# Kernel optimization log

Hardware: AMD Instinct MI355X
Metric: run time of the kernel (lower is better)

The kernel has to match this reference:

```python
import jax, jax.numpy as jnp
import numpy as np

C = 1024       # num_channels
HD = 64        # head_dim
NH = C // HD   # 16 heads
LMAX = 1024    # max segment length (static)
EPS = 1.1920929e-07  # torch.finfo(float32).eps, nn.RMSNorm default


def setup_inputs() -> dict:
    key = jax.random.key(0)
    ks = jax.random.split(key, 6)
    # 16 ragged segments, lengths alternate 768/256, sum = 8192
    lengths = np.tile(np.array([768, 256], dtype=np.int32), 8)
    cu = np.concatenate([[0], np.cumsum(lengths)]).astype(np.int32)
    T = int(cu[-1])
    s = 1.0 / np.sqrt(C)
    return {
        "x": jax.random.normal(ks[0], (T, C), jnp.float32),
        "cu_seqlens": jnp.asarray(cu),
        "Wq": jax.random.normal(ks[1], (C, C), jnp.float32) * s,
        "bq": jnp.zeros((C,), jnp.float32),
        "Wk": jax.random.normal(ks[2], (C, C), jnp.float32) * s,
        "bk": jnp.zeros((C,), jnp.float32),
        "Wv": jax.random.normal(ks[3], (C, C), jnp.float32) * s,
        "bv": jnp.zeros((C,), jnp.float32),
        "qn_w": jnp.ones((HD,), jnp.float32),
        "kn_w": jnp.ones((HD,), jnp.float32),
        "Wo": jax.random.normal(ks[4], (C, C), jnp.float32) * s,
        "bo": jnp.zeros((C,), jnp.float32),
    }


def _rmsnorm(h, w):
    # RMSNorm over last (head_dim) axis with learned scale
    return h * jax.lax.rsqrt(jnp.mean(h * h, axis=-1, keepdims=True) + EPS) * w


def reference(x, cu_seqlens, Wq, bq, Wk, bk, Wv, bv, qn_w, kn_w, Wo, bo):
    T = x.shape[0]
    q = (x @ Wq.T + bq).reshape(T, NH, HD)
    k = (x @ Wk.T + bk).reshape(T, NH, HD)
    v = (x @ Wv.T + bv).reshape(T, NH, HD)
    q = _rmsnorm(q, qn_w)
    k = _rmsnorm(k, kn_w)

    # gather ragged segments into padded [B, LMAX, H, D]
    starts = cu_seqlens[:-1]
    lens = cu_seqlens[1:] - starts
    pos = jnp.arange(LMAX, dtype=cu_seqlens.dtype)
    idx = starts[:, None] + pos[None, :]      # [B, LMAX]
    valid = pos[None, :] < lens[:, None]      # [B, LMAX]
    gidx = jnp.where(valid, idx, 0)
    qp, kp, vp = q[gidx], k[gidx], v[gidx]    # [B, LMAX, H, D]

    scale = 1.0 / np.sqrt(HD)
    scores = jnp.einsum('blhd,bshd->bhls', qp, kp) * scale
    scores = jnp.where(valid[:, None, None, :], scores, -1e9)  # mask pad keys
    probs = jax.nn.softmax(scores, axis=-1)
    op = jnp.einsum('bhls,bshd->blhd', probs, vp)  # [B, LMAX, H, D]

    # scatter valid tokens back to packed layout; pad rows dropped (idx=T OOB)
    sidx = jnp.where(valid, idx, T).reshape(-1)
    out = jnp.zeros((T, NH, HD), x.dtype).at[sidx].set(
        op.reshape(-1, NH, HD), mode='drop')
    return out.reshape(T, C) @ Wo.T + bo
```

## Files before the change

### kernel.cpp

```cpp
#include <hip/hip_runtime.h>

typedef unsigned short u16;
typedef unsigned int   u32;

typedef __bf16 bf16x8_t __attribute__((ext_vector_type(8)));
typedef bf16x8_t bf16x8 __attribute__((may_alias));
typedef float f32x4_t __attribute__((ext_vector_type(4)));
typedef f32x4_t f32x4 __attribute__((may_alias));
typedef u32 u32x4_t __attribute__((ext_vector_type(4)));
typedef u32x4_t u32x4 __attribute__((may_alias));
typedef u32 u32x2_t __attribute__((ext_vector_type(2)));
typedef u32x2_t u32x2 __attribute__((may_alias));

__device__ __forceinline__ u16 f2b(float f) {
  __bf16 h = (__bf16)f; u16 u; __builtin_memcpy(&u, &h, 2); return u;
}
__device__ __forceinline__ float b2f(u16 u) {
  u32 i = ((u32)u) << 16; float f; __builtin_memcpy(&f, &i, 4); return f;
}
__device__ __forceinline__ bf16x8_t cvt8(const float* p) {
  f32x4_t a = *(const f32x4*)p;
  f32x4_t b = *(const f32x4*)(p + 4);
  bf16x8_t v;
  v[0]=(__bf16)a[0]; v[1]=(__bf16)a[1]; v[2]=(__bf16)a[2]; v[3]=(__bf16)a[3];
  v[4]=(__bf16)b[0]; v[5]=(__bf16)b[1]; v[6]=(__bf16)b[2]; v[7]=(__bf16)b[3];
  return v;
}
typedef __attribute__((address_space(1))) const void* as1cv;
typedef __attribute__((address_space(3))) void* as3v;
__device__ __forceinline__ void gld16(const u16* g, u16* l) {
  __builtin_amdgcn_global_load_lds((as1cv)g, (as3v)l, 16, 0, 0);
}

#define EPS 1.1920929e-07f

#define WSZ (1024 * 1024)
__global__ __launch_bounds__(256) void cvt_pack(
    const float* __restrict__ x, const float* __restrict__ wq,
    const float* __restrict__ wk, const float* __restrict__ wv,
    const float* __restrict__ wo, u16* __restrict__ dst, int nx)
{
  int idx4 = blockIdx.x * 256 + threadIdx.x;
  const int total4 = (nx + 4 * WSZ) >> 2;
  for (; idx4 < total4; idx4 += gridDim.x * 256) {
    int i = idx4 << 2;
    const float* src;
    if (i < nx) src = x + i;
    else {
      int o = i - nx;
      if      (o <     WSZ) src = wq + o;
      else if (o < 2 * WSZ) src = wk + o - WSZ;
      else if (o < 3 * WSZ) src = wv + o - 2 * WSZ;
      else                  src = wo + o - 3 * WSZ;
    }
    f32x4_t v = *(const f32x4*)src;
    u32x2_t p;
    p[0] = (u32)f2b(v[0]) | ((u32)f2b(v[1]) << 16);
    p[1] = (u32)f2b(v[2]) | ((u32)f2b(v[3]) << 16);
    *(u32x2*)(dst + i) = p;
  }
}

#define BK 32
template<int NORM, int CF32>
__global__ __launch_bounds__(256, 2) void gemm_bt2(
    const u16* __restrict__ A, const u16* __restrict__ Bm,
    const float* __restrict__ bias0, const float* __restrict__ bias1, const float* __restrict__ bias2,
    const float* __restrict__ qn, const float* __restrict__ kn,
    void* __restrict__ C, int M, int K, int ldc)
{
  __shared__ alignas(16) u16 As[128 * BK];
  __shared__ alignas(16) u16 Bs[128 * BK];
  const int t = threadIdx.x;
  const int lane = t & 63, wave = t >> 6;
  const int quad = lane >> 4, col = lane & 15;
  const int m0 = blockIdx.x * 128, n0 = blockIdx.y * 128;
  const int seg = n0 >> 10, nl0 = n0 & 1023;
  const float* bias = seg == 0 ? bias0 : (seg == 1 ? bias1 : bias2);
  const int wm = (wave >> 1) * 64, wn = (wave & 1) * 64;

  const int lrow = t >> 2;
  const int lcol = (t & 3) * 8;
  const u16* ga0 = A  + (size_t)(m0 + lrow) * K + lcol;
  const u16* ga1 = A  + (size_t)(m0 + 64 + lrow) * K + lcol;
  const u16* gb0 = Bm + (size_t)(n0 + lrow) * K + lcol;
  const u16* gb1 = Bm + (size_t)(n0 + 64 + lrow) * K + lcol;
  u16* lA0 = As + t * 8;
  u16* lA1 = As + 64 * BK + t * 8;
  u16* lB0 = Bs + t * 8;
  u16* lB1 = Bs + 64 * BK + t * 8;

  f32x4_t acc[4][4] = {};
  for (int k0 = 0; k0 < K; k0 += BK) {
    __syncthreads();
    gld16(ga0 + k0, lA0);
    gld16(ga1 + k0, lA1);
    gld16(gb0 + k0, lB0);
    gld16(gb1 + k0, lB1);
    __syncthreads();
    bf16x8 af[4], bfr[4];
#pragma unroll
    for (int i = 0; i < 4; ++i) {
      af[i]  = *(const bf16x8*)(As + (wm + i * 16 + col) * BK + quad * 8);
      bfr[i] = *(const bf16x8*)(Bs + (wn + i * 16 + col) * BK + quad * 8);
    }
#pragma unroll
    for (int i = 0; i < 4; ++i)
#pragma unroll
      for (int j = 0; j < 4; ++j)
        acc[i][j] = __builtin_amdgcn_mfma_f32_16x16x32_bf16(af[i], bfr[j], acc[i][j], 0, 0, 0);
  }

  float bz[4], wz[4];
#pragma unroll
  for (int j = 0; j < 4; ++j) {
    bz[j] = bias[nl0 + wn + j * 16 + col];
    if (NORM) wz[j] = (seg == 0 ? qn : kn)[j * 16 + col];
  }
  const bool donorm = NORM && seg < 2;
#pragma unroll
  for (int i = 0; i < 4; ++i) {
#pragma unroll
    for (int rr = 0; rr < 4; ++rr) {
      int gm = m0 + wm + i * 16 + quad * 4 + rr;
      float v[4];
#pragma unroll
      for (int j = 0; j < 4; ++j) v[j] = acc[i][j][rr] + bz[j];
      if (donorm) {
        float ss = v[0]*v[0] + v[1]*v[1] + v[2]*v[2] + v[3]*v[3];
        ss += __shfl_xor(ss, 1);
        ss += __shfl_xor(ss, 2);
        ss += __shfl_xor(ss, 4);
        ss += __shfl_xor(ss, 8);
        float sc = rsqrtf(ss * (1.0f / 64.0f) + EPS);
#pragma unroll
        for (int j = 0; j < 4; ++j) v[j] *= sc * wz[j];
      }
      if (gm < M) {
#pragma unroll
        for (int j = 0; j < 4; ++j) {
          int gn = n0 + wn + j * 16 + col;
          if (CF32) ((float*)C)[(size_t)gm * ldc + gn] = v[j];
          else      ((u16*)C)[(size_t)gm * ldc + gn] = f2b(v[j]);
        }
      }
    }
  }
}

template<int AF32, int CF32>
__global__ __launch_bounds__(256, 2) void gemm_bt(
    const void* __restrict__ Av,
    const float* __restrict__ B0, const float* __restrict__ B1, const float* __restrict__ B2,
    const float* __restrict__ bias0, const float* __restrict__ bias1, const float* __restrict__ bias2,
    void* __restrict__ C, int M, int K, int ldc)
{
  __shared__ alignas(16) u16 As[128 * BK];
  __shared__ alignas(16) u16 Bs[128 * BK];
  const int t = threadIdx.x;
  const int lane = t & 63, wave = t >> 6;
  const int quad = lane >> 4, col = lane & 15;
  const int m0 = blockIdx.x * 128, n0 = blockIdx.y * 128;
  const int seg = n0 >> 10;
  const float* B    = seg == 0 ? B0    : (seg == 1 ? B1    : B2);
  const float* bias = seg == 0 ? bias0 : (seg == 1 ? bias1 : bias2);
  const int nl0 = n0 & 1023;
  const int wm = (wave >> 1) * 64, wn = (wave & 1) * 64;
  const int lrow = t >> 2;
  const int lcol = (t & 3) * 8;
  int ar0 = m0 + lrow;      if (ar0 >= M) ar0 = M - 1;
  int ar1 = m0 + 64 + lrow; if (ar1 >= M) ar1 = M - 1;
  const float* bp0 = B + (size_t)(nl0 + lrow) * K + lcol;
  const float* bp1 = B + (size_t)(nl0 + 64 + lrow) * K + lcol;
  const float* apf0 = (const float*)Av + (size_t)ar0 * K + lcol;
  const float* apf1 = (const float*)Av + (size_t)ar1 * K + lcol;
  const u16*   aph0 = (const u16*)Av   + (size_t)ar0 * K + lcol;
  const u16*   aph1 = (const u16*)Av   + (size_t)ar1 * K + lcol;
  u16* lA0 = As + t * 8;
  u16* lA1 = As + 64 * BK + t * 8;
  u16* lB0 = Bs + t * 8;
  u16* lB1 = Bs + 64 * BK + t * 8;

  f32x4_t acc[4][4] = {};
  for (int k0 = 0; k0 < K; k0 += BK) {
    bf16x8_t va0, va1, vb0, vb1;
    if (AF32) { va0 = cvt8(apf0 + k0); va1 = cvt8(apf1 + k0); }
    else {
      u32x4_t r0 = *(const u32x4*)(aph0 + k0);
      u32x4_t r1 = *(const u32x4*)(aph1 + k0);
      __builtin_memcpy(&va0, &r0, 16);
      __builtin_memcpy(&va1, &r1, 16);
    }
    vb0 = cvt8(bp0 + k0);
    vb1 = cvt8(bp1 + k0);
    __syncthreads();
    *(bf16x8*)lA0 = va0; *(bf16x8*)lA1 = va1;
    *(bf16x8*)lB0 = vb0; *(bf16x8*)lB1 = vb1;
    __syncthreads();
    bf16x8 af[4], bfr[4];
#pragma unroll
    for (int i = 0; i < 4; ++i) {
      af[i]  = *(const bf16x8*)(As + (wm + i * 16 + col) * BK + quad * 8);
      bfr[i] = *(const bf16x8*)(Bs + (wn + i * 16 + col) * BK + quad * 8);
    }
#pragma unroll
    for (int i = 0; i < 4; ++i)
#pragma unroll
      for (int j = 0; j < 4; ++j)
        acc[i][j] = __builtin_amdgcn_mfma_f32_16x16x32_bf16(af[i], bfr[j], acc[i][j], 0, 0, 0);
  }
#pragma unroll
  for (int j = 0; j < 4; ++j) {
    int gn = n0 + wn + j * 16 + col;
    float bz = bias[nl0 + wn + j * 16 + col];
#pragma unroll
    for (int i = 0; i < 4; ++i) {
#pragma unroll
      for (int rr = 0; rr < 4; ++rr) {
        int gm = m0 + wm + i * 16 + quad * 4 + rr;
        if (gm < M) {
          float v = acc[i][j][rr] + bz;
          if (CF32) ((float*)C)[(size_t)gm * ldc + gn] = v;
          else      ((u16*)C)[(size_t)gm * ldc + gn] = f2b(v);
        }
      }
    }
  }
}

__global__ __launch_bounds__(256) void rmsnorm_qk(
    u16* __restrict__ qkv, const float* __restrict__ qn, const float* __restrict__ kn, int T)
{
  int gid = blockIdx.x * 256 + threadIdx.x;
  int row = gid >> 4, sub = gid & 15;
  if (row >= 2 * T * 16) return;
  int which = row >= T * 16;
  int r = which ? row - T * 16 : row;
  int tok = r >> 4, head = r & 15;
  u16* p = qkv + (size_t)tok * 3072 + which * 1024 + head * 64 + sub * 4;
  u16 d0 = p[0], d1 = p[1], d2 = p[2], d3 = p[3];
  float f0 = b2f(d0), f1 = b2f(d1), f2v = b2f(d2), f3 = b2f(d3);
  float ss = f0 * f0 + f1 * f1 + f2v * f2v + f3 * f3;
  ss += __shfl_xor(ss, 1);
  ss += __shfl_xor(ss, 2);
  ss += __shfl_xor(ss, 4);
  ss += __shfl_xor(ss, 8);
  float sc = rsqrtf(ss * (1.0f / 64.0f) + EPS);
  const float* w = which ? kn : qn;
  p[0] = f2b(f0 * sc * w[sub * 4 + 0]);
  p[1] = f2b(f1 * sc * w[sub * 4 + 1]);
  p[2] = f2b(f2v * sc * w[sub * 4 + 2]);
  p[3] = f2b(f3 * sc * w[sub * 4 + 3]);
}

#define SKS 68
#define SVS 68
#define SPS 68
__global__ __launch_bounds__(256, 4) void attn_fwd(
    const u16* __restrict__ qkv, const int* __restrict__ cu, u16* __restrict__ out)
{
  __shared__ alignas(16) u16 Ks[64 * SKS];
  __shared__ alignas(16) u16 Vts[64 * SVS];
  __shared__ alignas(16) u16 Ps[8 * 16 * SPS];
  const int seq = blockIdx.z, head = blockIdx.x, qt = blockIdx.y;
  const int start = cu[seq], len = cu[seq + 1] - start;
  const int q0 = qt * 128;
  if (q0 >= len) return;
  const int t = threadIdx.x;
  const int lane = t & 63, wave = t >> 6, quad = lane >> 4, col = lane & 15;

  const int rA = q0 + wave * 16 + col, rB = rA + 64;
  const u16* qpA = qkv + (size_t)(start + (rA < len ? rA : len - 1)) * 3072 + head * 64 + quad * 8;
  const u16* qpB = qkv + (size_t)(start + (rB < len ? rB : len - 1)) * 3072 + head * 64 + quad * 8;
  bf16x8 qfA0 = *(const bf16x8*)qpA;
  bf16x8 qfA1 = *(const bf16x8*)(qpA + 32);
  bf16x8 qfB0 = *(const bf16x8*)qpB;
  bf16x8 qfB1 = *(const bf16x8*)(qpB + 32);

  f32x4_t accOA[4] = {}, accOB[4] = {};
  float lA[4] = {}, lB[4] = {};
  const float SC = 0.125f * 1.44269504089f;

  const int sp = t >> 3, dc = t & 7;
  const int kc = sp & 15, kh = sp >> 4;
  const int keyA = kc + 32 * kh;
  u16* ksA = Ks + keyA * SKS + dc * 8;
  u16* ksB = Ks + (keyA + 16) * SKS + dc * 8;
  const int vcol = kc * 4 + 2 * kh;
  const size_t kvbase = 1024 + head * 64 + dc * 8;

  const int nkv = (len + 63) >> 6;
  u32x4_t rkA, rkB, rvA, rvB;
  {
    int ta = start + (keyA      < len ? keyA      : len - 1);
    int tb = start + (keyA + 16 < len ? keyA + 16 : len - 1);
    const u16* pa = qkv + (size_t)ta * 3072 + kvbase;
    const u16* pb2 = qkv + (size_t)tb * 3072 + kvbase;
    rkA = *(const u32x4*)pa;   rvA = *(const u32x4*)(pa + 1024);
    rkB = *(const u32x4*)pb2;  rvB = *(const u32x4*)(pb2 + 1024);
  }

  for (int it = 0; it < nkv; ++it) {
    const int k0 = it << 6;
    __syncthreads();
    *(u32x4*)ksA = rkA;
    *(u32x4*)ksB = rkB;
    {
      const u16* a = (const u16*)&rvA;
      const u16* b = (const u16*)&rvB;
#pragma unroll
      for (int j = 0; j < 8; ++j) {
        u32 pk = (u32)a[j] | ((u32)b[j] << 16);
        *(u32*)(Vts + (dc * 8 + j) * SVS + vcol) = pk;
      }
    }
    __syncthreads();
    if (it + 1 < nkv) {
      int kb0 = k0 + 64;
      int ta = start + (kb0 + keyA      < len ? kb0 + keyA      : len - 1);
      int tb = start + (kb0 + keyA + 16 < len ? kb0 + keyA + 16 : len - 1);
      const u16* pa = qkv + (size_t)ta * 3072 + kvbase;
      const u16* pb2 = qkv + (size_t)tb * 3072 + kvbase;
      rkA = *(const u32x4*)pa;   rvA = *(const u32x4*)(pa + 1024);
      rkB = *(const u32x4*)pb2;  rvB = *(const u32x4*)(pb2 + 1024);
    }

    f32x4_t sgA[4], sgB[4];
#pragma unroll
    for (int g = 0; g < 4; ++g) {
      bf16x8 kb0 = *(const bf16x8*)(Ks + (g*16 + col) * SKS + quad * 8);
      bf16x8 kb1 = *(const bf16x8*)(Ks + (g*16 + col) * SKS + 32 + quad * 8);
      f32x4_t sA = {}, sB = {};
      sA = __builtin_amdgcn_mfma_f32_16x16x32_bf16(qfA0, kb0, sA, 0, 0, 0);
      sB = __builtin_amdgcn_mfma_f32_16x16x32_bf16(qfB0, kb0, sB, 0, 0, 0);
      sA = __builtin_amdgcn_mfma_f32_16x16x32_bf16(qfA1, kb1, sA, 0, 0, 0);
      sB = __builtin_amdgcn_mfma_f32_16x16x32_bf16(qfB1, kb1, sB, 0, 0, 0);
      sgA[g] = sA; sgB[g] = sB;
    }

    const bool full = (k0 + 64 <= len);
    bool vg[4];
#pragma unroll
    for (int g = 0; g < 4; ++g) vg[g] = full || (k0 + g*16 + col) < len;
    u16* pwA = Ps + wave * (16 * SPS);
    u16* pwB = Ps + (4 + wave) * (16 * SPS);
#pragma unroll
    for (int r = 0; r < 4; ++r) {
      u16 peA[4], peB[4];
#pragma unroll
      for (int g = 0; g < 4; ++g) {
        float pA = exp2f(sgA[g][r] * SC);
        float pB = exp2f(sgB[g][r] * SC);
        peA[g] = vg[g] ? f2b(pA) : (u16)0;
        peB[g] = vg[g] ? f2b(pB) : (u16)0;
      }
      lA[r] += (b2f(peA[0]) + b2f(peA[1])) + (b2f(peA[2]) + b2f(peA[3]));
      lB[r] += (b2f(peB[0]) + b2f(peB[1])) + (b2f(peB[2]) + b2f(peB[3]));
      u32x2_t wA, wB;
      wA[0] = (u32)peA[0] | ((u32)peA[1] << 16);
      wA[1] = (u32)peA[2] | ((u32)peA[3] << 16);
      wB[0] = (u32)peB[0] | ((u32)peB[1] << 16);
      wB[1] = (u32)peB[2] | ((u32)peB[3] << 16);
      *(u32x2*)(pwA + (quad*4 + r) * SPS + col * 4) = wA;
      *(u32x2*)(pwB + (quad*4 + r) * SPS + col * 4) = wB;
    }
    __threadfence_block();

    bf16x8 pfA0 = *(const bf16x8*)(pwA + col * SPS + quad * 8);
    bf16x8 pfA1 = *(const bf16x8*)(pwA + col * SPS + 32 + quad * 8);
    bf16x8 pfB0 = *(const bf16x8*)(pwB + col * SPS + quad * 8);
    bf16x8 pfB1 = *(const bf16x8*)(pwB + col * SPS + 32 + quad * 8);
#pragma unroll
    for (int c = 0; c < 4; ++c) {
      bf16x8 vf0 = *(const bf16x8*)(Vts + (c*16 + col) * SVS + quad * 8);
      bf16x8 vf1 = *(const bf16x8*)(Vts + (c*16 + col) * SVS + 32 + quad * 8);
      accOA[c] = __builtin_amdgcn_mfma_f32_16x16x32_bf16(pfA0, vf0, accOA[c], 0, 0, 0);
      accOB[c] = __builtin_amdgcn_mfma_f32_16x16x32_bf16(pfB0, vf0, accOB[c], 0, 0, 0);
      accOA[c] = __builtin_amdgcn_mfma_f32_16x16x32_bf16(pfA1, vf1, accOA[c], 0, 0, 0);
      accOB[c] = __builtin_amdgcn_mfma_f32_16x16x32_bf16(pfB1, vf1, accOB[c], 0, 0, 0);
    }
  }

#pragma unroll
  for (int r = 0; r < 4; ++r) {
    float sA = lA[r], sB = lB[r];
    sA += __shfl_xor(sA, 1); sB += __shfl_xor(sB, 1);
    sA += __shfl_xor(sA, 2); sB += __shfl_xor(sB, 2);
    sA += __shfl_xor(sA, 4); sB += __shfl_xor(sB, 4);
    sA += __shfl_xor(sA, 8); sB += __shfl_xor(sB, 8);
    int rowA = q0 + wave * 16 + quad * 4 + r;
    int rowB = rowA + 64;
    if (rowA < len) {
      float inv = 1.0f / sA;
      u16* op = out + (size_t)(start + rowA) * 1024 + head * 64 + col;
      op[0]  = f2b(accOA[0][r] * inv);
      op[16] = f2b(accOA[1][r] * inv);
      op[32] = f2b(accOA[2][r] * inv);
      op[48] = f2b(accOA[3][r] * inv);
    }
    if (rowB < len) {
      float inv = 1.0f / sB;
      u16* op = out + (size_t)(start + rowB) * 1024 + head * 64 + col;
      op[0]  = f2b(accOB[0][r] * inv);
      op[16] = f2b(accOB[1][r] * inv);
      op[32] = f2b(accOB[2][r] * inv);
      op[48] = f2b(accOB[3][r] * inv);
    }
  }
}

__global__ void ws_too_small_sentinel(float* out) {
  if (threadIdx.x == 0 && blockIdx.x == 0) out[0] = 1024.0f;
}

extern "C" void kernel_launch(void* const* d_in, const int* in_sizes, int n_in,
                              void* d_out, int out_size, void* d_ws, size_t ws_size,
                              hipStream_t stream) {
  const float* x  = (const float*)d_in[0];
  const int*   cu = (const int*)d_in[1];
  const float* Wq = (const float*)d_in[2];
  const float* bq = (const float*)d_in[3];
  const float* Wk = (const float*)d_in[4];
  const float* bk = (const float*)d_in[5];
  const float* Wv = (const float*)d_in[6];
  const float* bv = (const float*)d_in[7];
  const float* qn = (const float*)d_in[8];
  const float* kn = (const float*)d_in[9];
  const float* Wo = (const float*)d_in[10];
  const float* bo = (const float*)d_in[11];

  const int T = in_sizes[0] / 1024;
  const int nseq = in_sizes[1] - 1;

  const size_t need_fast = ((size_t)T * 5120 + 4 * WSZ) * 2;
  const size_t need_fall = (size_t)T * 4096 * 2;

  u16* qkv  = (u16*)d_ws;
  u16* attn = qkv + (size_t)T * 3072;
  dim3 blk(256);

  if (ws_size >= need_fast) {
    u16* xb   = attn + (size_t)T * 1024;
    u16* wqkv = xb + (size_t)T * 1024;
    u16* wo   = wqkv + 3 * WSZ;
    cvt_pack<<<dim3(1024), blk, 0, stream>>>(x, Wq, Wk, Wv, Wo, xb, T * 1024);
    gemm_bt2<1, 0><<<dim3((T + 127) / 128, 24), blk, 0, stream>>>(
        xb, wqkv, bq, bk, bv, qn, kn, qkv, T, 1024, 3072);
    attn_fwd<<<dim3(16, 8, nseq), blk, 0, stream>>>(qkv, cu, attn);
    gemm_bt2<0, 1><<<dim3((T + 127) / 128, 8), blk, 0, stream>>>(
        attn, wo, bo, bo, bo, qn, kn, d_out, T, 1024, 1024);
  } else if (ws_size >= need_fall) {
    gemm_bt<1, 0><<<dim3((T + 127) / 128, 24), blk, 0, stream>>>(
        x, Wq, Wk, Wv, bq, bk, bv, qkv, T, 1024, 3072);
    rmsnorm_qk<<<dim3((2 * T * 256 + 255) / 256), blk, 0, stream>>>(qkv, qn, kn, T);
    attn_fwd<<<dim3(16, 8, nseq), blk, 0, stream>>>(qkv, cu, attn);
    gemm_bt<0, 1><<<dim3((T + 127) / 128, 8), blk, 0, stream>>>(
        attn, Wo, Wo, Wo, bo, bo, bo, d_out, T, 1024, 1024);
  } else {
    ws_too_small_sentinel<<<1, 64, 0, stream>>>((float*)d_out);
  }
}
```

Measured before the change: 266.9 us.

## Replace bf16 GEMM with 256x256-tile, 8-wave, double-buffered swizzled-LDS kernel

Replaces the 128x128 tile, BK=32 GEMM with a 512-thread kernel that computes 256x256 output tiles using BK=64 K-steps. The next K-tile's global-to-LDS loads are double-buffered and interleaved with the MFMA phases. LDS columns are XOR-swizzled to avoid bank conflicts, and workgroup IDs are remapped for L2 locality. This targets the low arithmetic intensity and the exposed load latency of the old GEMM, at the cost of 128KB of LDS per block, heavy register use, and far fewer blocks: 32x12 for QKV and 32x4 for the output projection.

Result: slower. 288.3 us (+8.0%).

```diff
diff --git a/kernel.cpp b/kernel.cpp
--- a/kernel.cpp
+++ b/kernel.cpp
@@ -61,71 +61,118 @@
   }
 }
 
-#define BK 32
 template<int NORM, int CF32>
-__global__ __launch_bounds__(256, 2) void gemm_bt2(
+__global__ __launch_bounds__(512, 2) void gemm8(
     const u16* __restrict__ A, const u16* __restrict__ Bm,
     const float* __restrict__ bias0, const float* __restrict__ bias1, const float* __restrict__ bias2,
     const float* __restrict__ qn, const float* __restrict__ kn,
     void* __restrict__ C, int M, int K, int ldc)
 {
-  __shared__ alignas(16) u16 As[128 * BK];
-  __shared__ alignas(16) u16 Bs[128 * BK];
+  __shared__ alignas(16) u16 lds[65536];
   const int t = threadIdx.x;
   const int lane = t & 63, wave = t >> 6;
   const int quad = lane >> 4, col = lane & 15;
-  const int m0 = blockIdx.x * 128, n0 = blockIdx.y * 128;
-  const int seg = n0 >> 10, nl0 = n0 & 1023;
+  const int wm = wave >> 2, wn = wave & 3;
+
+  const int nwg = gridDim.x * gridDim.y;
+  int fid = blockIdx.y * gridDim.x + blockIdx.x;
+  int wg = (nwg & 7) ? fid : ((fid & 7) * (nwg >> 3) + (fid >> 3));
+  const int m0 = (wg % gridDim.x) * 256;
+  const int n0 = (wg / gridDim.x) * 256;
+
+  const int srow = t >> 3;
+  const int sx = ((t & 7) ^ (srow & 7)) << 3;
+  const u16* asrc[2][2];
+  const u16* bsrc[2][2];
+#pragma unroll
+  for (int h = 0; h < 2; ++h)
+#pragma unroll
+    for (int q = 0; q < 2; ++q) {
+      int ar = m0 + h * 128 + q * 64 + srow; if (ar >= M) ar = M - 1;
+      asrc[h][q] = A  + (size_t)ar * K + sx;
+      int br = n0 + h * 128 + q * 64 + srow;
+      bsrc[h][q] = Bm + (size_t)br * K + sx;
+    }
+  const int dst8 = t * 8;
+
+#pragma unroll
+  for (int h = 0; h < 2; ++h)
+#pragma unroll
+    for (int q = 0; q < 2; ++q) {
+      gld16(asrc[h][q],         lds +         h * 8192 + q * 4096 + dst8);
+      gld16(bsrc[h][q], lds + 32768 + h * 8192 + q * 4096 + dst8);
+    }
+  __syncthreads();
+
+  f32x4_t acc[8][4] = {};
+  const int nt = K >> 6;
+  for (int k = 0; k < nt; ++k) {
+    const int d = k & 1, nk = k + 1, nd = nk & 1;
+    const int koff = nk << 6;
+    const u16* Ab = lds +         (2 * d + wm) * 8192;
+    const u16* Bb = lds + 32768 + (2 * d + (wn >> 1)) * 8192;
+    const int browb = ((wn & 1) * 64) << 6;
+    bf16x8 bfr[4];
+#pragma unroll
+    for (int p = 0; p < 4; ++p) {
+      const int g = p & 1, ks = p >> 1;
+      const int ck = (((ks * 4 + quad) ^ (col & 7)) << 3);
+      if (g == 0) {
+#pragma unroll
+        for (int nj = 0; nj < 4; ++nj)
+          bfr[nj] = *(const bf16x8*)(Bb + browb + ((nj * 16 + col) << 6) + ck);
+      }
+      bf16x8 af[4];
+#pragma unroll
+      for (int i = 0; i < 4; ++i)
+        af[i] = *(const bf16x8*)(Ab + (((g * 4 + i) * 16 + col) << 6) + ck);
+      if (nk < nt) {
+        if (p == 0) {
+          gld16(asrc[0][0] + koff, lds + (2 * nd) * 8192 + dst8);
+          gld16(asrc[0][1] + koff, lds + (2 * nd) * 8192 + 4096 + dst8);
+        } else if (p == 1) {
+          gld16(asrc[1][0] + koff, lds + (2 * nd + 1) * 8192 + dst8);
+          gld16(asrc[1][1] + koff, lds + (2 * nd + 1) * 8192 + 4096 + dst8);
+        } else if (p == 2) {
+          gld16(bsrc[0][0] + koff, lds + 32768 + (2 * nd) * 8192 + dst8);
+          gld16(bsrc[0][1] + koff, lds + 32768 + (2 * nd) * 8192 + 4096 + dst8);
+        } else {
+          gld16(bsrc[1][0] + koff, lds + 32768 + (2 * nd + 1) * 8192 + dst8);
+          gld16(bsrc[1][1] + koff, lds + 32768 + (2 * nd + 1) * 8192 + 4096 + dst8);
+        }
+      }
+      __builtin_amdgcn_s_barrier();
+      __builtin_amdgcn_s_setprio(1);
+#pragma unroll
+      for (int i = 0; i < 4; ++i)
+#pragma unroll
+        for (int nj = 0; nj < 4; ++nj)
+          acc[g * 4 + i][nj] = __builtin_amdgcn_mfma_f32_16x16x32_bf16(
+              af[i], bfr[nj], acc[g * 4 + i][nj], 0, 0, 0);
+      __builtin_amdgcn_s_setprio(0);
+      if (p < 3) __builtin_amdgcn_s_barrier();
+    }
+    __syncthreads();
+  }
+
+  const int gnb = n0 + wn * 64;
+  const int seg = gnb >> 10, nl = gnb & 1023;
   const float* bias = seg == 0 ? bias0 : (seg == 1 ? bias1 : bias2);
-  const int wm = (wave >> 1) * 64, wn = (wave & 1) * 64;
-
-  const int lrow = t >> 2;
-  const int lcol = (t & 3) * 8;
-  const u16* ga0 = A  + (size_t)(m0 + lrow) * K + lcol;
-  const u16* ga1 = A  + (size_t)(m0 + 64 + lrow) * K + lcol;
-  const u16* gb0 = Bm + (size_t)(n0 + lrow) * K + lcol;
-  const u16* gb1 = Bm + (size_t)(n0 + 64 + lrow) * K + lcol;
-  u16* lA0 = As + t * 8;
-  u16* lA1 = As + 64 * BK + t * 8;
-  u16* lB0 = Bs + t * 8;
-  u16* lB1 = Bs + 64 * BK + t * 8;
-
-  f32x4_t acc[4][4] = {};
-  for (int k0 = 0; k0 < K; k0 += BK) {
-    __syncthreads();
-    gld16(ga0 + k0, lA0);
-    gld16(ga1 + k0, lA1);
-    gld16(gb0 + k0, lB0);
-    gld16(gb1 + k0, lB1);
-    __syncthreads();
-    bf16x8 af[4], bfr[4];
-#pragma unroll
-    for (int i = 0; i < 4; ++i) {
-      af[i]  = *(const bf16x8*)(As + (wm + i * 16 + col) * BK + quad * 8);
-      bfr[i] = *(const bf16x8*)(Bs + (wn + i * 16 + col) * BK + quad * 8);
-    }
-#pragma unroll
-    for (int i = 0; i < 4; ++i)
-#pragma unroll
-      for (int j = 0; j < 4; ++j)
-        acc[i][j] = __builtin_amdgcn_mfma_f32_16x16x32_bf16(af[i], bfr[j], acc[i][j], 0, 0, 0);
-  }
-
   float bz[4], wz[4];
 #pragma unroll
-  for (int j = 0; j < 4; ++j) {
-    bz[j] = bias[nl0 + wn + j * 16 + col];
-    if (NORM) wz[j] = (seg == 0 ? qn : kn)[j * 16 + col];
+  for (int nj = 0; nj < 4; ++nj) {
+    bz[nj] = bias[nl + nj * 16 + col];
+    if (NORM) wz[nj] = (seg == 0 ? qn : kn)[nj * 16 + col];
   }
   const bool donorm = NORM && seg < 2;
 #pragma unroll
-  for (int i = 0; i < 4; ++i) {
+  for (int mi = 0; mi < 8; ++mi) {
 #pragma unroll
     for (int rr = 0; rr < 4; ++rr) {
-      int gm = m0 + wm + i * 16 + quad * 4 + rr;
+      int gm = m0 + wm * 128 + mi * 16 + quad * 4 + rr;
       float v[4];
 #pragma unroll
-      for (int j = 0; j < 4; ++j) v[j] = acc[i][j][rr] + bz[j];
+      for (int nj = 0; nj < 4; ++nj) v[nj] = acc[mi][nj][rr] + bz[nj];
       if (donorm) {
         float ss = v[0]*v[0] + v[1]*v[1] + v[2]*v[2] + v[3]*v[3];
         ss += __shfl_xor(ss, 1);
@@ -134,20 +181,21 @@
         ss += __shfl_xor(ss, 8);
         float sc = rsqrtf(ss * (1.0f / 64.0f) + EPS);
 #pragma unroll
-        for (int j = 0; j < 4; ++j) v[j] *= sc * wz[j];
+        for (int nj = 0; nj < 4; ++nj) v[nj] *= sc * wz[nj];
       }
       if (gm < M) {
 #pragma unroll
-        for (int j = 0; j < 4; ++j) {
-          int gn = n0 + wn + j * 16 + col;
-          if (CF32) ((float*)C)[(size_t)gm * ldc + gn] = v[j];
-          else      ((u16*)C)[(size_t)gm * ldc + gn] = f2b(v[j]);
+        for (int nj = 0; nj < 4; ++nj) {
+          int gn = gnb + nj * 16 + col;
+          if (CF32) ((float*)C)[(size_t)gm * ldc + gn] = v[nj];
+          else      ((u16*)C)[(size_t)gm * ldc + gn] = f2b(v[nj]);
         }
       }
     }
   }
 }
 
+#define BK 32
 template<int AF32, int CF32>
 __global__ __launch_bounds__(256, 2) void gemm_bt(
     const void* __restrict__ Av,
@@ -444,10 +492,10 @@
     u16* wqkv = xb + (size_t)T * 1024;
     u16* wo   = wqkv + 3 * WSZ;
     cvt_pack<<<dim3(1024), blk, 0, stream>>>(x, Wq, Wk, Wv, Wo, xb, T * 1024);
-    gemm_bt2<1, 0><<<dim3((T + 127) / 128, 24), blk, 0, stream>>>(
+    gemm8<1, 0><<<dim3((T + 255) / 256, 12), dim3(512), 0, stream>>>(
         xb, wqkv, bq, bk, bv, qn, kn, qkv, T, 1024, 3072);
     attn_fwd<<<dim3(16, 8, nseq), blk, 0, stream>>>(qkv, cu, attn);
-    gemm_bt2<0, 1><<<dim3((T + 127) / 128, 8), blk, 0, stream>>>(
+    gemm8<0, 1><<<dim3((T + 255) / 256, 4), dim3(512), 0, stream>>>(
         attn, wo, bo, bo, bo, qn, kn, d_out, T, 1024, 1024);
   } else if (ws_size >= need_fall) {
     gemm_bt<1, 0><<<dim3((T + 127) / 128, 24), blk, 0, stream>>>(
```

## Add 256x256-tile 8-wave GEMM with async LDS double buffering for QKV projection

Applied to the files above, without the earlier changes.

Introduces a new GEMM kernel for the QKV projection. It uses 256x256 output tiles, 512 threads and a 64-wide K step, loads A and B directly into swizzled LDS in two buffers so the next stage overlaps with MFMA compute, and fuses bias plus per-head RMSNorm into the epilogue. The larger tiles give more data reuse per block and fewer blocks. The cost is 128KB of LDS, which limits occupancy, and a smaller grid (32x12 blocks) that may underfill the CUs.

Result: slower. 272.5 us (+2.1%).

```diff
diff --git a/kernel.cpp b/kernel.cpp
--- a/kernel.cpp
+++ b/kernel.cpp
@@ -58,6 +58,131 @@
     p[0] = (u32)f2b(v[0]) | ((u32)f2b(v[1]) << 16);
     p[1] = (u32)f2b(v[2]) | ((u32)f2b(v[3]) << 16);
     *(u32x2*)(dst + i) = p;
+  }
+}
+
+template<int NORM, int CF32>
+__global__ __launch_bounds__(512, 2) void gemm8(
+    const u16* __restrict__ A, const u16* __restrict__ Bm,
+    const float* __restrict__ bias0, const float* __restrict__ bias1, const float* __restrict__ bias2,
+    const float* __restrict__ qn, const float* __restrict__ kn,
+    void* __restrict__ C, int M, int K, int ldc)
+{
+  __shared__ alignas(16) u16 lds[65536];
+  const int t = threadIdx.x;
+  const int lane = t & 63, wave = t >> 6;
+  const int quad = lane >> 4, col = lane & 15;
+  const int wm = wave >> 2, wn = wave & 3;
+  const int m0 = blockIdx.x * 256, n0 = blockIdx.y * 256;
+
+  const int srow = t >> 3;
+  const int sx = ((t & 7) ^ (srow & 7)) << 3;
+  const u16* asrc[2][2];
+  const u16* bsrc[2][2];
+#pragma unroll
+  for (int h = 0; h < 2; ++h)
+#pragma unroll
+    for (int q = 0; q < 2; ++q) {
+      int ar = m0 + h * 128 + q * 64 + srow; if (ar >= M) ar = M - 1;
+      asrc[h][q] = A  + (size_t)ar * K + sx;
+      int br = n0 + h * 128 + q * 64 + srow;
+      bsrc[h][q] = Bm + (size_t)br * K + sx;
+    }
+  const int dst8 = t * 8;
+
+#define STAGE(kt, db) do {                                               \
+    const int koff_ = (kt) << 6;                                         \
+    gld16(asrc[0][0] + koff_, lds + (2*(db)    ) * 8192 + dst8);         \
+    gld16(asrc[0][1] + koff_, lds + (2*(db)    ) * 8192 + 4096 + dst8);  \
+    gld16(asrc[1][0] + koff_, lds + (2*(db) + 1) * 8192 + dst8);         \
+    gld16(asrc[1][1] + koff_, lds + (2*(db) + 1) * 8192 + 4096 + dst8);  \
+    gld16(bsrc[0][0] + koff_, lds + 32768 + (2*(db)    ) * 8192 + dst8); \
+    gld16(bsrc[0][1] + koff_, lds + 32768 + (2*(db)    ) * 8192 + 4096 + dst8); \
+    gld16(bsrc[1][0] + koff_, lds + 32768 + (2*(db) + 1) * 8192 + dst8); \
+    gld16(bsrc[1][1] + koff_, lds + 32768 + (2*(db) + 1) * 8192 + 4096 + dst8); \
+  } while (0)
+
+  STAGE(0, 0);
+
+  f32x4_t acc[8][4] = {};
+  const int nt = K >> 6;
+  for (int k = 0; k < nt; ++k) {
+    const int d = k & 1;
+    if (k + 1 < nt) {
+      STAGE(k + 1, d ^ 1);
+      asm volatile("s_waitcnt vmcnt(8)" ::: "memory");
+    } else {
+      asm volatile("s_waitcnt vmcnt(0)" ::: "memory");
+    }
+    asm volatile("s_barrier" ::: "memory");
+    const u16* Ab = lds +         (2 * d + wm) * 8192;
+    const u16* Bb = lds + 32768 + (2 * d + (wn >> 1)) * 8192;
+    const int browb = ((wn & 1) * 64) << 6;
+    bf16x8 bfr[4];
+#pragma unroll
+    for (int p = 0; p < 4; ++p) {
+      const int g = p & 1, ks = p >> 1;
+      const int ck = (((ks * 4 + quad) ^ (col & 7)) << 3);
+      if (g == 0) {
+#pragma unroll
+        for (int nj = 0; nj < 4; ++nj)
+          bfr[nj] = *(const bf16x8*)(Bb + browb + ((nj * 16 + col) << 6) + ck);
+      }
+      bf16x8 af[4];
+#pragma unroll
+      for (int i = 0; i < 4; ++i)
+        af[i] = *(const bf16x8*)(Ab + (((g * 4 + i) * 16 + col) << 6) + ck);
+      __builtin_amdgcn_s_setprio(1);
+#pragma unroll
+      for (int i = 0; i < 4; ++i)
+#pragma unroll
+        for (int nj = 0; nj < 4; ++nj)
+          acc[g * 4 + i][nj] = __builtin_amdgcn_mfma_f32_16x16x32_bf16(
+              af[i], bfr[nj], acc[g * 4 + i][nj], 0, 0, 0);
+      __builtin_amdgcn_s_setprio(0);
+    }
+    asm volatile("s_waitcnt lgkmcnt(0)" ::: "memory");
+    asm volatile("s_barrier" ::: "memory");
+  }
+#undef STAGE
+
+  const int gnb = n0 + wn * 64;
+  const int seg = gnb >> 10, nl = gnb & 1023;
+  const float* bias = seg == 0 ? bias0 : (seg == 1 ? bias1 : bias2);
+  float bz[4], wz[4];
+#pragma unroll
+  for (int nj = 0; nj < 4; ++nj) {
+    bz[nj] = bias[nl + nj * 16 + col];
+    if (NORM) wz[nj] = (seg == 0 ? qn : kn)[nj * 16 + col];
+  }
+  const bool donorm = NORM && seg < 2;
+#pragma unroll
+  for (int mi = 0; mi < 8; ++mi) {
+#pragma unroll
+    for (int rr = 0; rr < 4; ++rr) {
+      int gm = m0 + wm * 128 + mi * 16 + quad * 4 + rr;
+      float v[4];
+#pragma unroll
+      for (int nj = 0; nj < 4; ++nj) v[nj] = acc[mi][nj][rr] + bz[nj];
+      if (donorm) {
+        float ss = v[0]*v[0] + v[1]*v[1] + v[2]*v[2] + v[3]*v[3];
+        ss += __shfl_xor(ss, 1);
+        ss += __shfl_xor(ss, 2);
+        ss += __shfl_xor(ss, 4);
+        ss += __shfl_xor(ss, 8);
+        float sc = rsqrtf(ss * (1.0f / 64.0f) + EPS);
+#pragma unroll
+        for (int nj = 0; nj < 4; ++nj) v[nj] *= sc * wz[nj];
+      }
+      if (gm < M) {
+#pragma unroll
+        for (int nj = 0; nj < 4; ++nj) {
+          int gn = gnb + nj * 16 + col;
+          if (CF32) ((float*)C)[(size_t)gm * ldc + gn] = v[nj];
+          else      ((u16*)C)[(size_t)gm * ldc + gn] = f2b(v[nj]);
+        }
+      }
+    }
   }
 }
 
@@ -444,7 +569,7 @@
     u16* wqkv = xb + (size_t)T * 1024;
     u16* wo   = wqkv + 3 * WSZ;
     cvt_pack<<<dim3(1024), blk, 0, stream>>>(x, Wq, Wk, Wv, Wo, xb, T * 1024);
-    gemm_bt2<1, 0><<<dim3((T + 127) / 128, 24), blk, 0, stream>>>(
+    gemm8<1, 0><<<dim3((T + 255) / 256, 12), dim3(512), 0, stream>>>(
         xb, wqkv, bq, bk, bv, qn, kn, qkv, T, 1024, 3072);
     attn_fwd<<<dim3(16, 8, nseq), blk, 0, stream>>>(qkv, cu, attn);
     gemm_bt2<0, 1><<<dim3((T + 127) / 128, 8), blk, 0, stream>>>(
```
